# Kernel optimization log

Measured on AMD Instinct MI355X. Metric: run time of the kernel, lower is better.

Reference implementation:

```python
import jax, jax.numpy as jnp
import numpy as np

N_NODES = 100000
N_EDGES = 600000
HIDDEN = 128


def setup_inputs() -> dict:
    key = jax.random.key(0)
    ks = jax.random.split(key, 5)
    x = jax.random.normal(ks[0], (N_NODES, HIDDEN), dtype=jnp.float32)
    edge_index = jax.random.randint(ks[1], (2, N_EDGES), 0, N_NODES, dtype=jnp.int64)
    edge_weight = jax.random.uniform(ks[2], (N_EDGES,), dtype=jnp.float32)
    # MLP params: Linear(2*H+1 -> H), ReLU, Linear(H -> 1)
    W1 = jax.random.normal(ks[3], (2 * HIDDEN + 1, HIDDEN), dtype=jnp.float32) * (1.0 / np.sqrt(2 * HIDDEN + 1))
    b1 = jnp.zeros((HIDDEN,), dtype=jnp.float32)
    W2 = jax.random.normal(ks[4], (HIDDEN, 1), dtype=jnp.float32) * (1.0 / np.sqrt(HIDDEN))
    b2 = jnp.zeros((1,), dtype=jnp.float32)
    return {"x": x, "edge_index": edge_index, "edge_weight": edge_weight,
            "W1": W1, "b1": b1, "W2": W2, "b2": b2}


def reference(x, edge_index, edge_weight, W1, b1, W2, b2):
    num_nodes = x.shape[0]
    src = edge_index[0]
    tgt = edge_index[1]
    h_src = x[src]                      # [E, H] gather
    h_tgt = x[tgt]                      # [E, H] gather
    w = edge_weight[:, None]            # [E, 1]
    concat = jnp.concatenate([h_src, h_tgt, w], axis=-1)   # [E, 2H+1]
    hidden = jax.nn.relu(concat @ W1 + b1)                 # [E, H]
    scores = (hidden @ W2 + b2)[:, 0]                      # [E]
    # NOTE: the original _softmax_edge's max-pass uses index_put_(accumulate=True)
    # on a -inf buffer, so every touched entry stays -inf and is then replaced by 0;
    # the net effect is NO max subtraction. Faithful math: plain exp / segment_sum.
    exp_scores = jnp.exp(scores)
    sum_exp = jax.ops.segment_sum(exp_scores, tgt, num_segments=num_nodes)
    sum_exp = jnp.maximum(sum_exp, 1e-12)
    alpha = exp_scores / sum_exp[tgt]                      # [E]
    out = jax.ops.segment_sum(alpha[:, None] * h_src, tgt, num_segments=num_nodes)
    return x + out
```

## Files before the change

### kernel.cpp

```cpp
#include <hip/hip_runtime.h>
#include <hip/hip_bf16.h>

#define N_NODES 100000
#define N_EDGES 600000
#define HID 128
#define SCAN_NB 391
#define GEMM_BLOCKS 1563
#define FILL_BLOCKS 586


typedef short bf16x8 __attribute__((ext_vector_type(8)));
typedef float f32x4  __attribute__((ext_vector_type(4)));

__device__ inline unsigned short f2bf(float v) {
    __hip_bfloat16 h = __float2bfloat16(v);
    return *(unsigned short*)&h;
}
__device__ inline unsigned int pack2(float a, float b) {
    return (unsigned int)f2bf(a) | ((unsigned int)f2bf(b) << 16);
}
__device__ inline float2 bfpair(unsigned int u) {
    float lo = __uint_as_float(u << 16);
    float hi = __uint_as_float(u & 0xffff0000u);
    return make_float2(lo, hi);
}
__device__ inline void lds_barrier() {
    asm volatile("s_waitcnt lgkmcnt(0)" ::: "memory");
    __builtin_amdgcn_s_barrier();
}

__global__ __launch_bounds__(256) void k_prep(const float* __restrict__ W1,
                                              unsigned short* __restrict__ Bh,
                                              int* __restrict__ deg)
{
    int idx = blockIdx.x * 256 + threadIdx.x;
    if (idx < N_NODES) deg[idx] = 0;
    if (idx < 32768) {
        int n = idx & 255;
        int k = idx >> 8;
        float v = (n < HID) ? W1[k * HID + n] : W1[(HID + k) * HID + (n - HID)];
        Bh[(k >> 5) * 8192 + n * 32 + (k & 31)] = f2bf(v);
    }
}

__global__ __launch_bounds__(256) void k_count(const int* __restrict__ ei,
                                               int* __restrict__ deg)
{
    int e = blockIdx.x * blockDim.x + threadIdx.x;
    if (e < N_EDGES) atomicAdd(&deg[ei[N_EDGES + e]], 1);
}

__global__ __launch_bounds__(256) void k_rowptr(const int* __restrict__ deg,
                                                int* __restrict__ rowptr,
                                                int* __restrict__ cursor)
{
    __shared__ int s[256];
    int t = threadIdx.x;
    int b = blockIdx.x;
    int lim = b * 256;

    int acc = 0;
    for (int i = t; i < lim; i += 256) acc += deg[i];
    s[t] = acc;
    __syncthreads();
    #pragma unroll
    for (int off = 128; off > 0; off >>= 1) {
        if (t < off) s[t] += s[t + off];
        __syncthreads();
    }
    int pb = s[0];
    __syncthreads();

    int idx = lim + t;
    int v = (idx < N_NODES) ? deg[idx] : 0;
    s[t] = v;
    __syncthreads();
    #pragma unroll
    for (int off = 1; off < 256; off <<= 1) {
        int u = (t >= off) ? s[t - off] : 0;
        __syncthreads();
        s[t] += u;
        __syncthreads();
    }
    if (idx < N_NODES) {
        int r = pb + s[t] - v;
        rowptr[idx] = r;
        cursor[idx] = r;
    }
    if (idx == 0) rowptr[N_NODES] = N_EDGES;
}

__global__ __launch_bounds__(256) void k_gemm_fill(const float* __restrict__ x,
                                                   const unsigned short* __restrict__ BhG,
                                                   unsigned short* __restrict__ zbuf,
                                                   unsigned short* __restrict__ y2buf,
                                                   const int* __restrict__ ei,
                                                   const float* __restrict__ ew,
                                                   int* __restrict__ cursor,
                                                   uint2* __restrict__ eprs)
{
    __shared__ unsigned short Ah[64 * 128];

    if (blockIdx.x >= GEMM_BLOCKS) {
        int fb = blockIdx.x - GEMM_BLOCKS;
        for (int e = fb * 256 + threadIdx.x; e < N_EDGES; e += FILL_BLOCKS * 256) {
            int tgt = ei[N_EDGES + e];
            int pos = atomicAdd(&cursor[tgt], 1);
            eprs[pos] = make_uint2((unsigned int)ei[e], __float_as_uint(ew[e]));
        }
        return;
    }

    const int tid  = threadIdx.x;
    const int bm   = blockIdx.x * 64;
    const int wave = tid >> 6;
    const int lane = tid & 63;
    const int q    = lane >> 4;
    const int ln   = lane & 15;

    {
        const int r  = tid >> 2;
        const int c  = tid & 3;
        const int gm = bm + r;
        const bool ok = gm < N_NODES;
        const float* px = &x[(size_t)gm * HID + c * 32];

        float4 v0 = make_float4(0.f,0.f,0.f,0.f), v1=v0, v2=v0, v3=v0, v4=v0, v5=v0, v6=v0, v7=v0;
        if (ok) {
            v0 = *(const float4*)(px + 0);  v1 = *(const float4*)(px + 4);
            v2 = *(const float4*)(px + 8);  v3 = *(const float4*)(px + 12);
            v4 = *(const float4*)(px + 16); v5 = *(const float4*)(px + 20);
            v6 = *(const float4*)(px + 24); v7 = *(const float4*)(px + 28);
        }
        uint4 ch0, ch1, ch2, ch3;
        ch0.x = pack2(v0.x, v0.y); ch0.y = pack2(v0.z, v0.w); ch0.z = pack2(v1.x, v1.y); ch0.w = pack2(v1.z, v1.w);
        ch1.x = pack2(v2.x, v2.y); ch1.y = pack2(v2.z, v2.w); ch1.z = pack2(v3.x, v3.y); ch1.w = pack2(v3.z, v3.w);
        ch2.x = pack2(v4.x, v4.y); ch2.y = pack2(v4.z, v4.w); ch2.z = pack2(v5.x, v5.y); ch2.w = pack2(v5.z, v5.w);
        ch3.x = pack2(v6.x, v6.y); ch3.y = pack2(v6.z, v6.w); ch3.z = pack2(v7.x, v7.y); ch3.w = pack2(v7.z, v7.w);

        char* rowp = (char*)Ah + r * 256;
        const int swz = (r & 7) << 4;
        *(uint4*)(rowp + ((c * 64 +  0) ^ swz)) = ch0;
        *(uint4*)(rowp + ((c * 64 + 16) ^ swz)) = ch1;
        *(uint4*)(rowp + ((c * 64 + 32) ^ swz)) = ch2;
        *(uint4*)(rowp + ((c * 64 + 48) ^ swz)) = ch3;

        if (ok) {
            unsigned short* zp = &zbuf[(size_t)gm * 256 + 128 + c * 32];
            *(uint4*)(zp + 0)  = ch0;
            *(uint4*)(zp + 8)  = ch1;
            *(uint4*)(zp + 16) = ch2;
            *(uint4*)(zp + 24) = ch3;
        }
    }
    lds_barrier();

    bf16x8 ah[4][4];
    {
        const int swzr = (ln & 7) << 4;
        #pragma unroll
        for (int mt = 0; mt < 4; ++mt) {
            const char* rowp = (const char*)Ah + (mt * 16 + ln) * 256;
            #pragma unroll
            for (int ks = 0; ks < 4; ++ks) {
                ah[mt][ks] = *(const bf16x8*)(rowp + ((ks * 64 + q * 16) ^ swzr));
            }
        }
    }

    f32x4 acc[4][4] = {};
    #pragma unroll
    for (int nt = 0; nt < 4; ++nt) {
        bf16x8 bh[4];
        #pragma unroll
        for (int ks = 0; ks < 4; ++ks) {
            bh[ks] = *(const bf16x8*)&BhG[ks * 8192 + (wave * 64 + nt * 16 + ln) * 32 + q * 8];
        }
        #pragma unroll
        for (int mt = 0; mt < 4; ++mt) {
            #pragma unroll
            for (int ks = 0; ks < 4; ++ks) {
                acc[mt][nt] = __builtin_amdgcn_mfma_f32_16x16x32_bf16(bh[ks], ah[mt][ks], acc[mt][nt], 0, 0, 0);
            }
        }
    }

    #pragma unroll
    for (int mt = 0; mt < 4; ++mt) {
        int node = bm + mt * 16 + ln;
        if (node < N_NODES) {
            #pragma unroll
            for (int nt = 0; nt < 4; ++nt) {
                int col0 = wave * 64 + nt * 16 + q * 4;
                unsigned int lo = pack2(acc[mt][nt][0], acc[mt][nt][1]);
                unsigned int hi = pack2(acc[mt][nt][2], acc[mt][nt][3]);
                if (col0 < 128) *(uint2*)&zbuf[(size_t)node * 256 + col0] = make_uint2(lo, hi);
                else            *(uint2*)&y2buf[(size_t)node * 128 + (col0 - 128)] = make_uint2(lo, hi);
            }
        }
    }
}

__global__ __launch_bounds__(256) void k_fused(const unsigned int* __restrict__ zu,
                                               const unsigned int* __restrict__ y2u,
                                               const int* __restrict__ rowptr,
                                               const uint2* __restrict__ eprs,
                                               const float* __restrict__ x,
                                               const float* __restrict__ W1,
                                               const float* __restrict__ b1,
                                               const float* __restrict__ W2,
                                               const float* __restrict__ b2,
                                               float* __restrict__ out)
{
    int n = (blockIdx.x * blockDim.x + threadIdx.x) >> 6;
    int lane = threadIdx.x & 63;
    if (n >= N_NODES) return;
    int ql = lane & 15;
    int qi = lane >> 4;
    int c0 = ql * 8;

    uint4 uy2 = *(const uint4*)&y2u[(size_t)n * 64 + ql * 4];
    float2 y2a = bfpair(uy2.x), y2b = bfpair(uy2.y), y2c = bfpair(uy2.z), y2d = bfpair(uy2.w);
    float4 bv0 = *(const float4*)&b1[c0];
    float4 bv1 = *(const float4*)&b1[c0 + 4];
    float4 wr0 = *(const float4*)&W1[256 * HID + c0];
    float4 wr1 = *(const float4*)&W1[256 * HID + c0 + 4];
    float4 w20 = *(const float4*)&W2[c0];
    float4 w21 = *(const float4*)&W2[c0 + 4];
    float p0 = y2a.x + bv0.x, p1 = y2a.y + bv0.y, p2 = y2b.x + bv0.z, p3 = y2b.y + bv0.w;
    float p4 = y2c.x + bv1.x, p5 = y2c.y + bv1.y, p6 = y2d.x + bv1.z, p7 = y2d.y + bv1.w;
    float b2v = b2[0];

    int beg = rowptr[n], end = rowptr[n + 1];
    float a0 = 0.f, a1 = 0.f, a2 = 0.f, a3 = 0.f;
    float a4 = 0.f, a5 = 0.f, a6 = 0.f, a7 = 0.f;
    float denom = 0.f;

    for (int i = beg; i < end; i += 4) {
        int idx = i + qi;
        bool valid = idx < end;
        int ie = valid ? idx : (end - 1);
        uint2 ep = eprs[ie];
        size_t base = (size_t)ep.x * 128;
        float w = __uint_as_float(ep.y);
        uint4 uy = *(const uint4*)&zu[base + ql * 4];
        uint4 ux = *(const uint4*)&zu[base + 64 + ql * 4];

        float2 ya = bfpair(uy.x), yb = bfpair(uy.y), yc = bfpair(uy.z), yd = bfpair(uy.w);
        float h0 = fmaxf(fmaf(w, wr0.x, ya.x + p0), 0.f);
        float h1 = fmaxf(fmaf(w, wr0.y, ya.y + p1), 0.f);
        float h2 = fmaxf(fmaf(w, wr0.z, yb.x + p2), 0.f);
        float h3 = fmaxf(fmaf(w, wr0.w, yb.y + p3), 0.f);
        float h4 = fmaxf(fmaf(w, wr1.x, yc.x + p4), 0.f);
        float h5 = fmaxf(fmaf(w, wr1.y, yc.y + p5), 0.f);
        float h6 = fmaxf(fmaf(w, wr1.z, yd.x + p6), 0.f);
        float h7 = fmaxf(fmaf(w, wr1.w, yd.y + p7), 0.f);
        float s = ((h0 * w20.x + h1 * w20.y) + (h2 * w20.z + h3 * w20.w))
                + ((h4 * w21.x + h5 * w21.y) + (h6 * w21.z + h7 * w21.w));
        #pragma unroll
        for (int m = 1; m <= 8; m <<= 1) s += __shfl_xor(s, m, 64);
        float es = valid ? __expf(s + b2v) : 0.f;

        float2 xa = bfpair(ux.x), xb = bfpair(ux.y), xc = bfpair(ux.z), xd = bfpair(ux.w);
        a0 = fmaf(es, xa.x, a0); a1 = fmaf(es, xa.y, a1);
        a2 = fmaf(es, xb.x, a2); a3 = fmaf(es, xb.y, a3);
        a4 = fmaf(es, xc.x, a4); a5 = fmaf(es, xc.y, a5);
        a6 = fmaf(es, xd.x, a6); a7 = fmaf(es, xd.y, a7);
        denom += es;
    }

    #pragma unroll
    for (int m = 16; m <= 32; m <<= 1) {
        a0 += __shfl_xor(a0, m, 64); a1 += __shfl_xor(a1, m, 64);
        a2 += __shfl_xor(a2, m, 64); a3 += __shfl_xor(a3, m, 64);
        a4 += __shfl_xor(a4, m, 64); a5 += __shfl_xor(a5, m, 64);
        a6 += __shfl_xor(a6, m, 64); a7 += __shfl_xor(a7, m, 64);
        denom += __shfl_xor(denom, m, 64);
    }

    if (qi == 0) {
        float4 xt0 = *(const float4*)&x[(size_t)n * HID + c0];
        float4 xt1 = *(const float4*)&x[(size_t)n * HID + c0 + 4];
        float inv = 1.0f / fmaxf(denom, 1e-12f);
        float4 o0, o1;
        o0.x = xt0.x + a0 * inv; o0.y = xt0.y + a1 * inv;
        o0.z = xt0.z + a2 * inv; o0.w = xt0.w + a3 * inv;
        o1.x = xt1.x + a4 * inv; o1.y = xt1.y + a5 * inv;
        o1.z = xt1.z + a6 * inv; o1.w = xt1.w + a7 * inv;
        *(float4*)&out[(size_t)n * HID + c0]     = o0;
        *(float4*)&out[(size_t)n * HID + c0 + 4] = o1;
    }
}

extern "C" void kernel_launch(void* const* d_in, const int* in_sizes, int n_in,
                              void* d_out, int out_size, void* d_ws, size_t ws_size,
                              hipStream_t stream) {
    const float* x  = (const float*)d_in[0];
    const int*   ei = (const int*)d_in[1];
    const float* ew = (const float*)d_in[2];
    const float* W1 = (const float*)d_in[3];
    const float* b1 = (const float*)d_in[4];
    const float* W2 = (const float*)d_in[5];
    const float* b2 = (const float*)d_in[6];
    float* out = (float*)d_out;
    char* ws = (char*)d_ws;

    const size_t deg_b    = 400000;
    const size_t rowptr_b = 400016;
    const size_t cursor_b = 400000;
    const size_t eprs_b   = 4800000;
    const size_t part_b   = 1568;
    const size_t pb_b     = 1568;
    const size_t Bh_b     = 65536;

    char* p = ws;
    int* deg      = (int*)p;             p += deg_b;
    int* rowptr   = (int*)p;             p += rowptr_b;
    int* cursor   = (int*)p;             p += cursor_b;
    uint2* eprs   = (uint2*)p;           p += eprs_b;
    p += part_b;
    p += pb_b;
    unsigned short* BhG = (unsigned short*)p;  p += Bh_b;
    unsigned short* zbuf  = (unsigned short*)p;  p += (size_t)N_NODES * 256 * 2;
    unsigned short* y2buf = (unsigned short*)p;

    const int edge_blocks = (N_EDGES + 255) / 256;
    const int node_wave_blocks = (N_NODES * 64 + 255) / 256;

    hipLaunchKernelGGL(k_prep,   dim3(SCAN_NB), dim3(256), 0, stream, W1, BhG, deg);
    hipLaunchKernelGGL(k_count,  dim3(edge_blocks), dim3(256), 0, stream, ei, deg);
    hipLaunchKernelGGL(k_rowptr, dim3(SCAN_NB), dim3(256), 0, stream, deg, rowptr, cursor);
    hipLaunchKernelGGL(k_gemm_fill, dim3(GEMM_BLOCKS + FILL_BLOCKS), dim3(256), 0, stream,
                       x, BhG, zbuf, y2buf, ei, ew, cursor, eprs);
    hipLaunchKernelGGL(k_fused, dim3(node_wave_blocks), dim3(256), 0, stream,
                       (const unsigned int*)zbuf, (const unsigned int*)y2buf,
                       rowptr, eprs, x, W1, b1, W2, b2, out);
}
```

Before: 316.4 us.

## Overlap degree counting with GEMM and fill CSR via per-edge ranks

```diff
diff --git a/kernel.cpp b/kernel.cpp
--- a/kernel.cpp
+++ b/kernel.cpp
@@ -6,7 +6,7 @@
 #define HID 128
 #define SCAN_NB 391
 #define GEMM_BLOCKS 1563
-#define FILL_BLOCKS 586
+#define COUNT_BLOCKS 586
 
 
 typedef short bf16x8 __attribute__((ext_vector_type(8)));
@@ -29,84 +29,30 @@
     __builtin_amdgcn_s_barrier();
 }
 
-__global__ __launch_bounds__(256) void k_prep(const float* __restrict__ W1,
-                                              unsigned short* __restrict__ Bh,
-                                              int* __restrict__ deg)
+__global__ __launch_bounds__(256) void k_prepW1(const float* __restrict__ W1,
+                                                unsigned short* __restrict__ Bh)
 {
     int idx = blockIdx.x * 256 + threadIdx.x;
-    if (idx < N_NODES) deg[idx] = 0;
-    if (idx < 32768) {
-        int n = idx & 255;
-        int k = idx >> 8;
-        float v = (n < HID) ? W1[k * HID + n] : W1[(HID + k) * HID + (n - HID)];
-        Bh[(k >> 5) * 8192 + n * 32 + (k & 31)] = f2bf(v);
-    }
-}
-
-__global__ __launch_bounds__(256) void k_count(const int* __restrict__ ei,
-                                               int* __restrict__ deg)
-{
-    int e = blockIdx.x * blockDim.x + threadIdx.x;
-    if (e < N_EDGES) atomicAdd(&deg[ei[N_EDGES + e]], 1);
-}
-
-__global__ __launch_bounds__(256) void k_rowptr(const int* __restrict__ deg,
-                                                int* __restrict__ rowptr,
-                                                int* __restrict__ cursor)
-{
-    __shared__ int s[256];
-    int t = threadIdx.x;
-    int b = blockIdx.x;
-    int lim = b * 256;
-
-    int acc = 0;
-    for (int i = t; i < lim; i += 256) acc += deg[i];
-    s[t] = acc;
-    __syncthreads();
-    #pragma unroll
-    for (int off = 128; off > 0; off >>= 1) {
-        if (t < off) s[t] += s[t + off];
-        __syncthreads();
-    }
-    int pb = s[0];
-    __syncthreads();
-
-    int idx = lim + t;
-    int v = (idx < N_NODES) ? deg[idx] : 0;
-    s[t] = v;
-    __syncthreads();
-    #pragma unroll
-    for (int off = 1; off < 256; off <<= 1) {
-        int u = (t >= off) ? s[t - off] : 0;
-        __syncthreads();
-        s[t] += u;
-        __syncthreads();
-    }
-    if (idx < N_NODES) {
-        int r = pb + s[t] - v;
-        rowptr[idx] = r;
-        cursor[idx] = r;
-    }
-    if (idx == 0) rowptr[N_NODES] = N_EDGES;
-}
-
-__global__ __launch_bounds__(256) void k_gemm_fill(const float* __restrict__ x,
-                                                   const unsigned short* __restrict__ BhG,
-                                                   unsigned short* __restrict__ zbuf,
-                                                   unsigned short* __restrict__ y2buf,
-                                                   const int* __restrict__ ei,
-                                                   const float* __restrict__ ew,
-                                                   int* __restrict__ cursor,
-                                                   uint2* __restrict__ eprs)
+    int n = idx & 255;
+    int k = idx >> 8;
+    float v = (n < HID) ? W1[k * HID + n] : W1[(HID + k) * HID + (n - HID)];
+    Bh[(k >> 5) * 8192 + n * 32 + (k & 31)] = f2bf(v);
+}
+
+__global__ __launch_bounds__(256) void k_gemm_count(const float* __restrict__ x,
+                                                    const unsigned short* __restrict__ BhG,
+                                                    unsigned short* __restrict__ zbuf,
+                                                    unsigned short* __restrict__ y2buf,
+                                                    const int* __restrict__ ei,
+                                                    int* __restrict__ deg,
+                                                    int* __restrict__ rank)
 {
     __shared__ unsigned short Ah[64 * 128];
 
     if (blockIdx.x >= GEMM_BLOCKS) {
-        int fb = blockIdx.x - GEMM_BLOCKS;
-        for (int e = fb * 256 + threadIdx.x; e < N_EDGES; e += FILL_BLOCKS * 256) {
-            int tgt = ei[N_EDGES + e];
-            int pos = atomicAdd(&cursor[tgt], 1);
-            eprs[pos] = make_uint2((unsigned int)ei[e], __float_as_uint(ew[e]));
+        int cb = blockIdx.x - GEMM_BLOCKS;
+        for (int e = cb * 256 + threadIdx.x; e < N_EDGES; e += COUNT_BLOCKS * 256) {
+            rank[e] = atomicAdd(&deg[ei[N_EDGES + e]], 1);
         }
         return;
     }
@@ -198,6 +144,54 @@
                 else            *(uint2*)&y2buf[(size_t)node * 128 + (col0 - 128)] = make_uint2(lo, hi);
             }
         }
+    }
+}
+
+__global__ __launch_bounds__(256) void k_rowptr(const int* __restrict__ deg,
+                                                int* __restrict__ rowptr)
+{
+    __shared__ int s[256];
+    int t = threadIdx.x;
+    int b = blockIdx.x;
+    int lim = b * 256;
+
+    int acc = 0;
+    for (int i = t; i < lim; i += 256) acc += deg[i];
+    s[t] = acc;
+    __syncthreads();
+    #pragma unroll
+    for (int off = 128; off > 0; off >>= 1) {
+        if (t < off) s[t] += s[t + off];
+        __syncthreads();
+    }
+    int pb = s[0];
+    __syncthreads();
+
+    int idx = lim + t;
+    int v = (idx < N_NODES) ? deg[idx] : 0;
+    s[t] = v;
+    __syncthreads();
+    #pragma unroll
+    for (int off = 1; off < 256; off <<= 1) {
+        int u = (t >= off) ? s[t - off] : 0;
+        __syncthreads();
+        s[t] += u;
+        __syncthreads();
+    }
+    if (idx < N_NODES) rowptr[idx] = pb + s[t] - v;
+    if (idx == 0) rowptr[N_NODES] = N_EDGES;
+}
+
+__global__ __launch_bounds__(256) void k_fill(const int* __restrict__ ei,
+                                              const float* __restrict__ ew,
+                                              const int* __restrict__ rowptr,
+                                              const int* __restrict__ rank,
+                                              uint2* __restrict__ eprs)
+{
+    for (int e = blockIdx.x * 256 + threadIdx.x; e < N_EDGES; e += COUNT_BLOCKS * 256) {
+        int tgt = ei[N_EDGES + e];
+        int pos = rowptr[tgt] + rank[e];
+        eprs[pos] = make_uint2((unsigned int)ei[e], __float_as_uint(ew[e]));
     }
 }
 
@@ -307,32 +301,28 @@
 
     const size_t deg_b    = 400000;
     const size_t rowptr_b = 400016;
-    const size_t cursor_b = 400000;
+    const size_t rank_b   = 2400000;
     const size_t eprs_b   = 4800000;
-    const size_t part_b   = 1568;
-    const size_t pb_b     = 1568;
     const size_t Bh_b     = 65536;
 
     char* p = ws;
     int* deg      = (int*)p;             p += deg_b;
     int* rowptr   = (int*)p;             p += rowptr_b;
-    int* cursor   = (int*)p;             p += cursor_b;
+    int* rank     = (int*)p;             p += rank_b;
     uint2* eprs   = (uint2*)p;           p += eprs_b;
-    p += part_b;
-    p += pb_b;
     unsigned short* BhG = (unsigned short*)p;  p += Bh_b;
     unsigned short* zbuf  = (unsigned short*)p;  p += (size_t)N_NODES * 256 * 2;
     unsigned short* y2buf = (unsigned short*)p;
 
-    const int edge_blocks = (N_EDGES + 255) / 256;
     const int node_wave_blocks = (N_NODES * 64 + 255) / 256;
 
-    hipLaunchKernelGGL(k_prep,   dim3(SCAN_NB), dim3(256), 0, stream, W1, BhG, deg);
-    hipLaunchKernelGGL(k_count,  dim3(edge_blocks), dim3(256), 0, stream, ei, deg);
-    hipLaunchKernelGGL(k_rowptr, dim3(SCAN_NB), dim3(256), 0, stream, deg, rowptr, cursor);
-    hipLaunchKernelGGL(k_gemm_fill, dim3(GEMM_BLOCKS + FILL_BLOCKS), dim3(256), 0, stream,
-                       x, BhG, zbuf, y2buf, ei, ew, cursor, eprs);
-    hipLaunchKernelGGL(k_fused, dim3(node_wave_blocks), dim3(256), 0, stream,
+    hipMemsetAsync(deg, 0, 400000, stream);
+    hipLaunchKernelGGL(k_prepW1, dim3(128), dim3(256), 0, stream, W1, BhG);
+    hipLaunchKernelGGL(k_gemm_count, dim3(GEMM_BLOCKS + COUNT_BLOCKS), dim3(256), 0, stream,
+                       x, BhG, zbuf, y2buf, ei, deg, rank);
+    hipLaunchKernelGGL(k_rowptr, dim3(SCAN_NB), dim3(256), 0, stream, deg, rowptr);
+    hipLaunchKernelGGL(k_fill,   dim3(COUNT_BLOCKS), dim3(256), 0, stream, ei, ew, rowptr, rank, eprs);
+    hipLaunchKernelGGL(k_fused,  dim3(node_wave_blocks), dim3(256), 0, stream,
                        (const unsigned int*)zbuf, (const unsigned int*)y2buf,
                        rowptr, eprs, x, W1, b1, W2, b2, out);
 }
```

Result: faster. 301.2 us (-4.8%).
